# Optimization experiments

Hardware: AMD Instinct MI355X
Metric: run time of the kernel (lower is better)

The kernel has to match this reference:

```python
import jax, jax.numpy as jnp
import numpy as np

P, F_IN, HG, C, T, E, HOUT = 4096, 64, 64, 64, 32, 65536, 12
LEAKY_SLOPE = 0.2
LN_EPS = 1e-5


def setup_inputs() -> dict:
    key = jax.random.key(0)
    ks = jax.random.split(key, 14)
    g = lambda k, shape, scale: (jax.random.normal(k, shape, jnp.float32) * scale)
    return {
        "X": jax.random.normal(ks[0], (1, P, F_IN, T), jnp.float32),
        "edge_index": jax.random.randint(ks[1], (T, 2, E), 0, P, jnp.int32),
        # GATv2 params (single head)
        "Wl": g(ks[2], (F_IN, HG), 0.1),
        "Wr": g(ks[3], (F_IN, HG), 0.1),
        "att": g(ks[4], (HG,), 0.1),
        "gat_b": g(ks[5], (HG,), 0.02),
        # 1x1 time conv (HG -> C) and 1x1 residual conv (F_IN -> C)
        "W_time": g(ks[6], (C, HG), 0.1),
        "b_time": g(ks[7], (C,), 0.02),
        "W_res": g(ks[8], (C, F_IN), 0.1),
        "b_res": g(ks[9], (C,), 0.02),
        # LayerNorm over channel dim C
        "ln_g": jnp.ones((C,), jnp.float32),
        "ln_b": jnp.zeros((C,), jnp.float32),
        # final conv: Conv2d(in=T, out=HOUT, kernel=(1, C)) -> weight (HOUT, T, C)
        "W_final": g(ks[10], (HOUT, T, C), 0.05),
        "b_final": g(ks[11], (HOUT,), 0.02),
    }


def reference(X, edge_index, Wl, Wr, att, gat_b, W_time, b_time, W_res, b_res,
              ln_g, ln_b, W_final, b_final):
    Pn = X.shape[1]

    def gat_t(x, edges):
        # x: (P, F_IN), edges: (2, E) with edges[0]=src j, edges[1]=dst i
        src, dst = edges[0], edges[1]
        hl = x @ Wl                      # (P, HG) messages
        hr = x @ Wr                      # (P, HG) query side
        e = jax.nn.leaky_relu(hl[src] + hr[dst], LEAKY_SLOPE) @ att  # (E,)
        emax = jax.ops.segment_max(e, dst, num_segments=Pn)
        ex = jnp.exp(e - emax[dst])
        den = jax.ops.segment_sum(ex, dst, num_segments=Pn)
        alpha = ex / den[dst]            # softmax over in-edges of each dst
        return jax.ops.segment_sum(alpha[:, None] * hl[src], dst,
                                   num_segments=Pn) + gat_b  # (P, HG)

    xs = jnp.moveaxis(X[0], -1, 0)                     # (T, P, F_IN)
    X_hat = jax.nn.relu(jax.vmap(gat_t)(xs, edge_index))  # (T, P, HG)

    th = jnp.einsum('tph,ch->tpc', X_hat, W_time) + b_time  # time conv 1x1
    rs = jnp.einsum('tpf,cf->tpc', xs, W_res) + b_res       # residual conv 1x1
    y = jax.nn.relu(th + rs)                                 # (T, P, C)

    mu = jnp.mean(y, axis=-1, keepdims=True)
    var = jnp.var(y, axis=-1, keepdims=True)
    yn = (y - mu) * jax.lax.rsqrt(var + LN_EPS) * ln_g + ln_b  # (T, P, C)

    # final conv: in-channels = T, kernel (1, C) -> contract over t and c
    out = jnp.einsum('tpc,otc->po', yn, W_final) + b_final     # (P, HOUT)
    return out[None]                                           # (1, P, HOUT)
```

## Files before the change

### kernel.cpp

```cpp
#include <hip/hip_runtime.h>
#include <math.h>

#define NP 4096
#define F_IN 64
#define HG 64
#define NC 64
#define NT 32
#define NE 65536
#define HOUT 12
#define LEAKY 0.2f
#define LN_EPS 1e-5f
#define CAPC 32
#define XSP 2568

template <int CTRL>
__device__ __forceinline__ float dppadd(float v, float x) {
    int r = __builtin_amdgcn_update_dpp(0, __builtin_bit_cast(int, x), CTRL, 0xF, 0xF, false);
    return v + __builtin_bit_cast(float, r);
}
__device__ __forceinline__ float rowsum16(float v) {
    v = dppadd<0x128>(v, v);
    v = dppadd<0x124>(v, v);
    v = dppadd<0x122>(v, v);
    v = dppadd<0x121>(v, v);
    return v;
}
__device__ __forceinline__ float laneXorSum(float v) {
    v += __shfl_xor(v, 16, 64);
    v += __shfl_xor(v, 32, 64);
    return v;
}

#define FMA4(Acomp, B, r)                                                     \
    acc[r][0] += (Acomp) * (B).x; acc[r][1] += (Acomp) * (B).y;               \
    acc[r][2] += (Acomp) * (B).z; acc[r][3] += (Acomp) * (B).w;

__global__ __launch_bounds__(256) void k_front(const float* __restrict__ X,
        const float* __restrict__ Wl, const float* __restrict__ Wr,
        const float* __restrict__ W_res, const float* __restrict__ b_res,
        const float* __restrict__ bf,
        const int* __restrict__ EI,
        float* __restrict__ hl, float* __restrict__ hr, float* __restrict__ rs,
        float* __restrict__ out,
        int* __restrict__ cnt, unsigned short* __restrict__ scap) {
    __shared__ float smem[9488];
    int b = blockIdx.x;
    int tid = threadIdx.x;
    if (b < 512) {
        unsigned short (*buck)[CAPC] = (unsigned short (*)[CAPC])smem;
        int* cnts = (int*)(smem + 8192);
        int t = (b & 7) + 8 * ((b >> 3) & 3);
        int rem = b >> 5;
        int c = rem & 1, r = rem >> 1;
        cnts[tid] = 0; cnts[tid + 256] = 0;
        __syncthreads();
        const int4* srcA = (const int4*)(EI + (size_t)t * 2 * NE) + c * (NE / 8);
        const int4* dstA = (const int4*)(EI + (size_t)t * 2 * NE + NE) + c * (NE / 8);
        for (int i = tid; i < NE / 8; i += 256) {
            int4 s = srcA[i];
            int4 d = dstA[i];
            if ((d.x >> 9) == r) { int lo = d.x & 511; int sl = atomicAdd(&cnts[lo], 1); if (sl < CAPC) buck[lo][sl] = (unsigned short)s.x; }
            if ((d.y >> 9) == r) { int lo = d.y & 511; int sl = atomicAdd(&cnts[lo], 1); if (sl < CAPC) buck[lo][sl] = (unsigned short)s.y; }
            if ((d.z >> 9) == r) { int lo = d.z & 511; int sl = atomicAdd(&cnts[lo], 1); if (sl < CAPC) buck[lo][sl] = (unsigned short)s.z; }
            if ((d.w >> 9) == r) { int lo = d.w & 511; int sl = atomicAdd(&cnts[lo], 1); if (sl < CAPC) buck[lo][sl] = (unsigned short)s.w; }
        }
        __syncthreads();
        int obase = ((t * 2 + c) << 12) + (r << 9);
        cnt[obase + tid] = cnts[tid];
        cnt[obase + tid + 256] = cnts[tid + 256];
        unsigned int* dstw = (unsigned int*)(scap + (size_t)obase * CAPC);
        const unsigned int* srcw = (const unsigned int*)buck;
        for (int i = tid; i < 512 * CAPC / 2; i += 256)
            dstw[i] = srcw[i];
    } else if (b < 2560) {
        float* xs = smem;
        float (*bk)[68] = (float (*)[68])(smem + 2 * XSP);
        int p0 = (b - 512) * 2;
        const float4* Xp = (const float4*)(X + (size_t)p0 * F_IN * NT);
        for (int i4 = tid; i4 < 1024; i4 += 256) {
            int pp = i4 >> 9, f = (i4 >> 3) & 63, t0 = (i4 & 7) * 4;
            *(float4*)&xs[pp * XSP + f * 40 + t0] = Xp[i4];
        }
        int ng = tid & 15, pp = (tid >> 4) & 1, tg = tid >> 5;
        int n0 = ng * 4, t0 = tg * 4;
        int ppb = pp * XSP;
        {
            const float4* B4 = (const float4*)Wl;
            for (int i4 = tid; i4 < 1024; i4 += 256)
                *(float4*)&bk[i4 >> 4][(i4 & 15) * 4] = B4[i4];
            __syncthreads();
            float acc[4][4];
#pragma unroll
            for (int i = 0; i < 4; ++i)
#pragma unroll
                for (int j2 = 0; j2 < 4; ++j2) acc[i][j2] = 0.f;
#pragma unroll 8
            for (int f = 0; f < F_IN; ++f) {
                float4 B = *(const float4*)&bk[f][n0];
                float4 A = *(const float4*)&xs[ppb + f * 40 + t0];
                FMA4(A.x, B, 0) FMA4(A.y, B, 1) FMA4(A.z, B, 2) FMA4(A.w, B, 3)
            }
#pragma unroll
            for (int i = 0; i < 4; ++i) {
                float4 v;
                v.x = acc[i][0]; v.y = acc[i][1]; v.z = acc[i][2]; v.w = acc[i][3];
                *(float4*)&hl[((size_t)(t0 + i) * NP + p0 + pp) * HG + n0] = v;
            }
            __syncthreads();
        }
        {
            const float4* B4 = (const float4*)Wr;
            for (int i4 = tid; i4 < 1024; i4 += 256)
                *(float4*)&bk[i4 >> 4][(i4 & 15) * 4] = B4[i4];
            __syncthreads();
            float acc[4][4];
#pragma unroll
            for (int i = 0; i < 4; ++i)
#pragma unroll
                for (int j2 = 0; j2 < 4; ++j2) acc[i][j2] = 0.f;
#pragma unroll 8
            for (int f = 0; f < F_IN; ++f) {
                float4 B = *(const float4*)&bk[f][n0];
                float4 A = *(const float4*)&xs[ppb + f * 40 + t0];
                FMA4(A.x, B, 0) FMA4(A.y, B, 1) FMA4(A.z, B, 2) FMA4(A.w, B, 3)
            }
#pragma unroll
            for (int i = 0; i < 4; ++i) {
                float4 v;
                v.x = acc[i][0]; v.y = acc[i][1]; v.z = acc[i][2]; v.w = acc[i][3];
                *(float4*)&hr[((size_t)(t0 + i) * NP + p0 + pp) * HG + n0] = v;
            }
            __syncthreads();
        }
        {
            for (int i = tid; i < F_IN * NC; i += 256) {
                int c = i >> 6, f = i & 63;
                bk[f][c] = W_res[i];
            }
            __syncthreads();
            float4 br4 = *(const float4*)&b_res[n0];
            float acc[4][4];
#pragma unroll
            for (int i = 0; i < 4; ++i) {
                acc[i][0] = br4.x; acc[i][1] = br4.y; acc[i][2] = br4.z; acc[i][3] = br4.w;
            }
#pragma unroll 8
            for (int f = 0; f < F_IN; ++f) {
                float4 B = *(const float4*)&bk[f][n0];
                float4 A = *(const float4*)&xs[ppb + f * 40 + t0];
                FMA4(A.x, B, 0) FMA4(A.y, B, 1) FMA4(A.z, B, 2) FMA4(A.w, B, 3)
            }
#pragma unroll
            for (int i = 0; i < 4; ++i) {
                float4 v;
                v.x = acc[i][0]; v.y = acc[i][1]; v.z = acc[i][2]; v.w = acc[i][3];
                *(float4*)&rs[((size_t)(t0 + i) * NP + p0 + pp) * NC + n0] = v;
            }
        }
    } else {
        int i = (b - 2560) * 256 + tid;
        out[i] = bf[i % HOUT];
    }
}

__global__ __launch_bounds__(256, 8) void k_gat(const float* __restrict__ hl,
        float* __restrict__ hr,
        const int* __restrict__ cnt, const unsigned short* __restrict__ scap,
        const float* __restrict__ att, const float* __restrict__ gat_b) {
    __shared__ int sidx[4][72];
    int b = blockIdx.x;
    int k = b >> 3;
    int t = (b & 7) + 8 * (k >> 10);
    int ws = __builtin_amdgcn_readfirstlane(threadIdx.x >> 6);
    int i = (k & 1023) * 4 + ws;
    int lane = threadIdx.x & 63;
    int row = lane >> 4;
    int c0 = (lane & 15) * 4;
    const float* hlt = hl + (size_t)t * NP * HG;
    float4 at4 = *(const float4*)&att[c0];
    int d0 = cnt[((t * 2 + 0) << 12) + i]; d0 = (d0 < CAPC) ? d0 : CAPC;
    int d1 = cnt[((t * 2 + 1) << 12) + i]; d1 = (d1 < CAPC) ? d1 : CAPC;
    int deg = d0 + d1;
    const unsigned short* s0p = scap + ((size_t)(((t * 2 + 0) << 12) + i)) * CAPC;
    const unsigned short* s1p = scap + ((size_t)(((t * 2 + 1) << 12) + i)) * CAPC;
    int li = (lane < deg) ? lane : 0;
    int f1 = (li >= d0);
    int idx = f1 ? (li - d0) : li;
    sidx[ws][lane] = (int)(f1 ? s1p : s0p)[idx];
    if (lane < 8) sidx[ws][64 + lane] = 0;
    size_t nbase = ((size_t)t * NP + i) * HG;
    float4 r4 = *(const float4*)&hr[nbase + c0];
    int degp = (deg + 7) & ~7;
    float l = 0.f;
    float4 acc = {0.f, 0.f, 0.f, 0.f};
    float4 h0, h1;
    {
        int sa = sidx[ws][row];
        int sb = sidx[ws][4 + row];
        h0 = *(const float4*)&hlt[((size_t)sa << 6) + c0];
        h1 = *(const float4*)&hlt[((size_t)sb << 6) + c0];
    }
    for (int j = 0; j < degp; j += 8) {
        int na = sidx[ws][j + 8 + row];
        int nb = sidx[ws][j + 12 + row];
        float4 hn0 = *(const float4*)&hlt[((size_t)na << 6) + c0];
        float4 hn1 = *(const float4*)&hlt[((size_t)nb << 6) + c0];
        float4 z0, z1;
        z0.x = h0.x + r4.x; z0.y = h0.y + r4.y; z0.z = h0.z + r4.z; z0.w = h0.w + r4.w;
        z1.x = h1.x + r4.x; z1.y = h1.y + r4.y; z1.z = h1.z + r4.z; z1.w = h1.w + r4.w;
        z0.x = fmaxf(z0.x, LEAKY * z0.x); z0.y = fmaxf(z0.y, LEAKY * z0.y);
        z0.z = fmaxf(z0.z, LEAKY * z0.z); z0.w = fmaxf(z0.w, LEAKY * z0.w);
        z1.x = fmaxf(z1.x, LEAKY * z1.x); z1.y = fmaxf(z1.y, LEAKY * z1.y);
        z1.z = fmaxf(z1.z, LEAKY * z1.z); z1.w = fmaxf(z1.w, LEAKY * z1.w);
        float e0 = rowsum16(z0.x * at4.x + z0.y * at4.y + z0.z * at4.z + z0.w * at4.w);
        float e1 = rowsum16(z1.x * at4.x + z1.y * at4.y + z1.z * at4.z + z1.w * at4.w);
        float w0 = __expf(e0);
        float w1 = __expf(e1);
        w0 = (j + row < deg) ? w0 : 0.f;
        w1 = (j + 4 + row < deg) ? w1 : 0.f;
        l += w0 + w1;
        acc.x += w0 * h0.x + w1 * h1.x;
        acc.y += w0 * h0.y + w1 * h1.y;
        acc.z += w0 * h0.z + w1 * h1.z;
        acc.w += w0 * h0.w + w1 * h1.w;
        h0 = hn0; h1 = hn1;
    }
    float lt = laneXorSum(l);
    acc.x = laneXorSum(acc.x);
    acc.y = laneXorSum(acc.y);
    acc.z = laneXorSum(acc.z);
    acc.w = laneXorSum(acc.w);
    if (row == 0) {
        float inv = (deg > 0) ? (1.0f / lt) : 0.f;
        float4 gb = *(const float4*)&gat_b[c0];
        float4 o;
        o.x = fmaxf(acc.x * inv + gb.x, 0.f);
        o.y = fmaxf(acc.y * inv + gb.y, 0.f);
        o.z = fmaxf(acc.z * inv + gb.z, 0.f);
        o.w = fmaxf(acc.w * inv + gb.w, 0.f);
        *(float4*)&hr[nbase + c0] = o;
    }
}

__global__ __launch_bounds__(256) void k_pf(const float* __restrict__ Xhat,
        const float* __restrict__ W_time, const float* __restrict__ b_time,
        const float* __restrict__ rs, const float* __restrict__ ln_g,
        const float* __restrict__ ln_b, const float* __restrict__ Wf,
        float* __restrict__ out) {
    __shared__ float in_t[64][68];
    __shared__ float bk[64][68];
    int bx = blockIdx.x;
    int tc = bx & 7;
    int p0 = (bx >> 3) * 64;
    int tid = threadIdx.x;
    for (int i = tid; i < 4096; i += 256)
        bk[i & 63][i >> 6] = W_time[i];
    int cg = tid & 15, pg = tid >> 4;
    int c0 = cg * 4, pl = pg * 4;
    float4 bt4 = *(const float4*)&b_time[c0];
    float4 lg = *(const float4*)&ln_g[c0];
    float4 lb = *(const float4*)&ln_b[c0];
    float ot[4][HOUT];
#pragma unroll
    for (int i = 0; i < 4; ++i)
#pragma unroll
        for (int o = 0; o < HOUT; ++o) ot[i][o] = 0.f;
    float4 rg[4];
    {
        const float4* src = (const float4*)(Xhat + ((size_t)tc * NP + p0) * HG);
#pragma unroll
        for (int r = 0; r < 4; ++r) rg[r] = src[tid + 256 * r];
    }
    for (int ti = 0; ti < 4; ++ti) {
        int t = tc + ti * 8;
        __syncthreads();
#pragma unroll
        for (int r = 0; r < 4; ++r) {
            int i4 = tid + 256 * r;
            *(float4*)&in_t[i4 >> 4][(i4 & 15) * 4] = rg[r];
        }
        __syncthreads();
        if (ti < 3) {
            const float4* src = (const float4*)(Xhat + ((size_t)(t + 8) * NP + p0) * HG);
#pragma unroll
            for (int r = 0; r < 4; ++r) rg[r] = src[tid + 256 * r];
        }
        float acc[4][4];
#pragma unroll
        for (int i = 0; i < 4; ++i) {
            acc[i][0] = bt4.x; acc[i][1] = bt4.y; acc[i][2] = bt4.z; acc[i][3] = bt4.w;
        }
#pragma unroll
        for (int k4 = 0; k4 < 16; ++k4) {
            float4 A0 = *(const float4*)&in_t[pl + 0][k4 * 4];
            float4 A1 = *(const float4*)&in_t[pl + 1][k4 * 4];
            float4 A2 = *(const float4*)&in_t[pl + 2][k4 * 4];
            float4 A3 = *(const float4*)&in_t[pl + 3][k4 * 4];
            float4 B0 = *(const float4*)&bk[k4 * 4 + 0][c0];
            FMA4(A0.x, B0, 0) FMA4(A1.x, B0, 1) FMA4(A2.x, B0, 2) FMA4(A3.x, B0, 3)
            float4 B1 = *(const float4*)&bk[k4 * 4 + 1][c0];
            FMA4(A0.y, B1, 0) FMA4(A1.y, B1, 1) FMA4(A2.y, B1, 2) FMA4(A3.y, B1, 3)
            float4 B2 = *(const float4*)&bk[k4 * 4 + 2][c0];
            FMA4(A0.z, B2, 0) FMA4(A1.z, B2, 1) FMA4(A2.z, B2, 2) FMA4(A3.z, B2, 3)
            float4 B3 = *(const float4*)&bk[k4 * 4 + 3][c0];
            FMA4(A0.w, B3, 0) FMA4(A1.w, B3, 1) FMA4(A2.w, B3, 2) FMA4(A3.w, B3, 3)
        }
        float4 ynv[4];
#pragma unroll
        for (int i = 0; i < 4; ++i) {
            size_t prow = (size_t)t * NP + p0 + pl + i;
            float4 r4 = *(const float4*)&rs[prow * NC + c0];
            float y0 = fmaxf(acc[i][0] + r4.x, 0.f), y1 = fmaxf(acc[i][1] + r4.y, 0.f);
            float y2 = fmaxf(acc[i][2] + r4.z, 0.f), y3 = fmaxf(acc[i][3] + r4.w, 0.f);
            float s = rowsum16(y0 + y1 + y2 + y3);
            float ss = rowsum16(y0 * y0 + y1 * y1 + y2 * y2 + y3 * y3);
            float mu = s * (1.f / 64.f);
            float var = ss * (1.f / 64.f) - mu * mu;
            float rsd = rsqrtf(var + LN_EPS);
            ynv[i].x = (y0 - mu) * rsd * lg.x + lb.x;
            ynv[i].y = (y1 - mu) * rsd * lg.y + lb.y;
            ynv[i].z = (y2 - mu) * rsd * lg.z + lb.z;
            ynv[i].w = (y3 - mu) * rsd * lg.w + lb.w;
        }
#pragma unroll
        for (int o = 0; o < HOUT; ++o) {
            float4 w4 = *(const float4*)&Wf[(size_t)o * NT * NC + t * NC + c0];
#pragma unroll
            for (int i = 0; i < 4; ++i)
                ot[i][o] += ynv[i].x * w4.x + ynv[i].y * w4.y
                          + ynv[i].z * w4.z + ynv[i].w * w4.w;
        }
    }
#pragma unroll
    for (int i = 0; i < 4; ++i)
#pragma unroll
        for (int o = 0; o < HOUT; ++o) ot[i][o] = rowsum16(ot[i][o]);
    if (cg == 0) {
#pragma unroll
        for (int i = 0; i < 4; ++i) {
            int p = p0 + pl + i;
#pragma unroll
            for (int o = 0; o < HOUT; ++o)
                atomicAdd(&out[p * HOUT + o], ot[i][o]);
        }
    }
}

extern "C" void kernel_launch(void* const* d_in, const int* in_sizes, int n_in,
                              void* d_out, int out_size, void* d_ws, size_t ws_size,
                              hipStream_t stream) {
    const float* X      = (const float*)d_in[0];
    const int*   EI     = (const int*)d_in[1];
    const float* Wl     = (const float*)d_in[2];
    const float* Wr     = (const float*)d_in[3];
    const float* att    = (const float*)d_in[4];
    const float* gat_b  = (const float*)d_in[5];
    const float* W_time = (const float*)d_in[6];
    const float* b_time = (const float*)d_in[7];
    const float* W_res  = (const float*)d_in[8];
    const float* b_res  = (const float*)d_in[9];
    const float* ln_g   = (const float*)d_in[10];
    const float* ln_b   = (const float*)d_in[11];
    const float* Wf     = (const float*)d_in[12];
    const float* bf     = (const float*)d_in[13];
    float* out = (float*)d_out;

    char* ws = (char*)d_ws;
    const size_t MB = 1024 * 1024;
    float* hl   = (float*)(ws);
    float* hr   = (float*)(ws + 32 * MB);
    float* rs   = (float*)(ws + 64 * MB);
    int*   cnt  = (int*)  (ws + 96 * MB);
    unsigned short* scap = (unsigned short*)(ws + 97 * MB);

    k_front<<<2752, 256, 0, stream>>>(X, Wl, Wr, W_res, b_res, bf, EI,
                                      hl, hr, rs, out, cnt, scap);
    k_gat  <<<(NT * NP) / 4, 256, 0, stream>>>(hl, hr, cnt, scap, att, gat_b);
    k_pf   <<<512, 256, 0, stream>>>(hr, W_time, b_time, rs, ln_g, ln_b, Wf, out);
}
```

Before: 273.0 us.

## Fuse GAT aggregation into post-GAT time-conv/LayerNorm/final-conv kernel

Merges the GAT attention kernel and the post-processing kernel into one. Each block computes GAT outputs for 64 nodes at a given timestep straight into shared memory, then applies the time conv, residual, LayerNorm and final projection. This drops the global round trip of X_hat and one kernel launch. The cost is fewer blocks (1024 instead of 32768 GAT blocks) and serial per-wave node loops, so there is less parallelism for hiding gather latency.

Result: slower. 331.2 us (+21.3%).

```diff
diff --git a/kernel.cpp b/kernel.cpp
--- a/kernel.cpp
+++ b/kernel.cpp
@@ -163,128 +163,107 @@
     }
 }
 
-__global__ __launch_bounds__(256, 8) void k_gat(const float* __restrict__ hl,
-        float* __restrict__ hr,
+__global__ __launch_bounds__(256) void k_gpf(const float* __restrict__ hl,
+        const float* __restrict__ hr, const float* __restrict__ rs,
         const int* __restrict__ cnt, const unsigned short* __restrict__ scap,
-        const float* __restrict__ att, const float* __restrict__ gat_b) {
-    __shared__ int sidx[4][72];
-    int b = blockIdx.x;
-    int k = b >> 3;
-    int t = (b & 7) + 8 * (k >> 10);
-    int ws = __builtin_amdgcn_readfirstlane(threadIdx.x >> 6);
-    int i = (k & 1023) * 4 + ws;
-    int lane = threadIdx.x & 63;
-    int row = lane >> 4;
-    int c0 = (lane & 15) * 4;
-    const float* hlt = hl + (size_t)t * NP * HG;
-    float4 at4 = *(const float4*)&att[c0];
-    int d0 = cnt[((t * 2 + 0) << 12) + i]; d0 = (d0 < CAPC) ? d0 : CAPC;
-    int d1 = cnt[((t * 2 + 1) << 12) + i]; d1 = (d1 < CAPC) ? d1 : CAPC;
-    int deg = d0 + d1;
-    const unsigned short* s0p = scap + ((size_t)(((t * 2 + 0) << 12) + i)) * CAPC;
-    const unsigned short* s1p = scap + ((size_t)(((t * 2 + 1) << 12) + i)) * CAPC;
-    int li = (lane < deg) ? lane : 0;
-    int f1 = (li >= d0);
-    int idx = f1 ? (li - d0) : li;
-    sidx[ws][lane] = (int)(f1 ? s1p : s0p)[idx];
-    if (lane < 8) sidx[ws][64 + lane] = 0;
-    size_t nbase = ((size_t)t * NP + i) * HG;
-    float4 r4 = *(const float4*)&hr[nbase + c0];
-    int degp = (deg + 7) & ~7;
-    float l = 0.f;
-    float4 acc = {0.f, 0.f, 0.f, 0.f};
-    float4 h0, h1;
-    {
-        int sa = sidx[ws][row];
-        int sb = sidx[ws][4 + row];
-        h0 = *(const float4*)&hlt[((size_t)sa << 6) + c0];
-        h1 = *(const float4*)&hlt[((size_t)sb << 6) + c0];
-    }
-    for (int j = 0; j < degp; j += 8) {
-        int na = sidx[ws][j + 8 + row];
-        int nb = sidx[ws][j + 12 + row];
-        float4 hn0 = *(const float4*)&hlt[((size_t)na << 6) + c0];
-        float4 hn1 = *(const float4*)&hlt[((size_t)nb << 6) + c0];
-        float4 z0, z1;
-        z0.x = h0.x + r4.x; z0.y = h0.y + r4.y; z0.z = h0.z + r4.z; z0.w = h0.w + r4.w;
-        z1.x = h1.x + r4.x; z1.y = h1.y + r4.y; z1.z = h1.z + r4.z; z1.w = h1.w + r4.w;
-        z0.x = fmaxf(z0.x, LEAKY * z0.x); z0.y = fmaxf(z0.y, LEAKY * z0.y);
-        z0.z = fmaxf(z0.z, LEAKY * z0.z); z0.w = fmaxf(z0.w, LEAKY * z0.w);
-        z1.x = fmaxf(z1.x, LEAKY * z1.x); z1.y = fmaxf(z1.y, LEAKY * z1.y);
-        z1.z = fmaxf(z1.z, LEAKY * z1.z); z1.w = fmaxf(z1.w, LEAKY * z1.w);
-        float e0 = rowsum16(z0.x * at4.x + z0.y * at4.y + z0.z * at4.z + z0.w * at4.w);
-        float e1 = rowsum16(z1.x * at4.x + z1.y * at4.y + z1.z * at4.z + z1.w * at4.w);
-        float w0 = __expf(e0);
-        float w1 = __expf(e1);
-        w0 = (j + row < deg) ? w0 : 0.f;
-        w1 = (j + 4 + row < deg) ? w1 : 0.f;
-        l += w0 + w1;
-        acc.x += w0 * h0.x + w1 * h1.x;
-        acc.y += w0 * h0.y + w1 * h1.y;
-        acc.z += w0 * h0.z + w1 * h1.z;
-        acc.w += w0 * h0.w + w1 * h1.w;
-        h0 = hn0; h1 = hn1;
-    }
-    float lt = laneXorSum(l);
-    acc.x = laneXorSum(acc.x);
-    acc.y = laneXorSum(acc.y);
-    acc.z = laneXorSum(acc.z);
-    acc.w = laneXorSum(acc.w);
-    if (row == 0) {
-        float inv = (deg > 0) ? (1.0f / lt) : 0.f;
-        float4 gb = *(const float4*)&gat_b[c0];
-        float4 o;
-        o.x = fmaxf(acc.x * inv + gb.x, 0.f);
-        o.y = fmaxf(acc.y * inv + gb.y, 0.f);
-        o.z = fmaxf(acc.z * inv + gb.z, 0.f);
-        o.w = fmaxf(acc.w * inv + gb.w, 0.f);
-        *(float4*)&hr[nbase + c0] = o;
-    }
-}
-
-__global__ __launch_bounds__(256) void k_pf(const float* __restrict__ Xhat,
+        const float* __restrict__ att, const float* __restrict__ gat_b,
         const float* __restrict__ W_time, const float* __restrict__ b_time,
-        const float* __restrict__ rs, const float* __restrict__ ln_g,
-        const float* __restrict__ ln_b, const float* __restrict__ Wf,
-        float* __restrict__ out) {
+        const float* __restrict__ ln_g, const float* __restrict__ ln_b,
+        const float* __restrict__ Wf, float* __restrict__ out) {
     __shared__ float in_t[64][68];
     __shared__ float bk[64][68];
+    __shared__ int sidx[4][72];
     int bx = blockIdx.x;
-    int tc = bx & 7;
-    int p0 = (bx >> 3) * 64;
+    int tc = bx & 15;
+    int p0 = (bx >> 4) * 64;
     int tid = threadIdx.x;
+    int ws = __builtin_amdgcn_readfirstlane(tid >> 6);
+    int lane = tid & 63;
+    int row = lane >> 4;
+    int cg = lane & 15;
+    int c0 = cg * 4;
     for (int i = tid; i < 4096; i += 256)
         bk[i & 63][i >> 6] = W_time[i];
-    int cg = tid & 15, pg = tid >> 4;
-    int c0 = cg * 4, pl = pg * 4;
+    float4 at4 = *(const float4*)&att[c0];
+    float4 gb4 = *(const float4*)&gat_b[c0];
     float4 bt4 = *(const float4*)&b_time[c0];
-    float4 lg = *(const float4*)&ln_g[c0];
-    float4 lb = *(const float4*)&ln_b[c0];
+    float4 lg  = *(const float4*)&ln_g[c0];
+    float4 lb  = *(const float4*)&ln_b[c0];
+    int pg = tid >> 4, pl = pg * 4;
     float ot[4][HOUT];
 #pragma unroll
     for (int i = 0; i < 4; ++i)
 #pragma unroll
         for (int o = 0; o < HOUT; ++o) ot[i][o] = 0.f;
-    float4 rg[4];
-    {
-        const float4* src = (const float4*)(Xhat + ((size_t)tc * NP + p0) * HG);
-#pragma unroll
-        for (int r = 0; r < 4; ++r) rg[r] = src[tid + 256 * r];
-    }
-    for (int ti = 0; ti < 4; ++ti) {
-        int t = tc + ti * 8;
+
+    for (int ti = 0; ti < 2; ++ti) {
+        int t = tc + 16 * ti;
+        const float* hlt = hl + (size_t)t * NP * HG;
+        for (int q = 0; q < 16; ++q) {
+            int plocal = ws * 16 + q;
+            int p = p0 + plocal;
+            int d0 = cnt[((t * 2 + 0) << 12) + p]; d0 = (d0 < CAPC) ? d0 : CAPC;
+            int d1 = cnt[((t * 2 + 1) << 12) + p]; d1 = (d1 < CAPC) ? d1 : CAPC;
+            int deg = d0 + d1;
+            const unsigned short* s0p = scap + ((size_t)(((t * 2 + 0) << 12) + p)) * CAPC;
+            const unsigned short* s1p = scap + ((size_t)(((t * 2 + 1) << 12) + p)) * CAPC;
+            int li = (lane < deg) ? lane : 0;
+            int f1 = (li >= d0);
+            int idx = f1 ? (li - d0) : li;
+            sidx[ws][lane] = (int)(f1 ? s1p : s0p)[idx];
+            if (lane < 8) sidx[ws][64 + lane] = 0;
+            float4 r4 = *(const float4*)&hr[((size_t)t * NP + p) * HG + c0];
+            int degp = (deg + 7) & ~7;
+            float l = 0.f;
+            float4 acc = {0.f, 0.f, 0.f, 0.f};
+            float4 h0, h1;
+            {
+                int sa = sidx[ws][row];
+                int sb = sidx[ws][4 + row];
+                h0 = *(const float4*)&hlt[((size_t)sa << 6) + c0];
+                h1 = *(const float4*)&hlt[((size_t)sb << 6) + c0];
+            }
+            for (int j = 0; j < degp; j += 8) {
+                int na = sidx[ws][j + 8 + row];
+                int nb = sidx[ws][j + 12 + row];
+                float4 hn0 = *(const float4*)&hlt[((size_t)na << 6) + c0];
+                float4 hn1 = *(const float4*)&hlt[((size_t)nb << 6) + c0];
+                float4 z0, z1;
+                z0.x = h0.x + r4.x; z0.y = h0.y + r4.y; z0.z = h0.z + r4.z; z0.w = h0.w + r4.w;
+                z1.x = h1.x + r4.x; z1.y = h1.y + r4.y; z1.z = h1.z + r4.z; z1.w = h1.w + r4.w;
+                z0.x = fmaxf(z0.x, LEAKY * z0.x); z0.y = fmaxf(z0.y, LEAKY * z0.y);
+                z0.z = fmaxf(z0.z, LEAKY * z0.z); z0.w = fmaxf(z0.w, LEAKY * z0.w);
+                z1.x = fmaxf(z1.x, LEAKY * z1.x); z1.y = fmaxf(z1.y, LEAKY * z1.y);
+                z1.z = fmaxf(z1.z, LEAKY * z1.z); z1.w = fmaxf(z1.w, LEAKY * z1.w);
+                float e0 = rowsum16(z0.x * at4.x + z0.y * at4.y + z0.z * at4.z + z0.w * at4.w);
+                float e1 = rowsum16(z1.x * at4.x + z1.y * at4.y + z1.z * at4.z + z1.w * at4.w);
+                float w0 = __expf(e0);
+                float w1 = __expf(e1);
+                w0 = (j + row < deg) ? w0 : 0.f;
+                w1 = (j + 4 + row < deg) ? w1 : 0.f;
+                l += w0 + w1;
+                acc.x += w0 * h0.x + w1 * h1.x;
+                acc.y += w0 * h0.y + w1 * h1.y;
+                acc.z += w0 * h0.z + w1 * h1.z;
+                acc.w += w0 * h0.w + w1 * h1.w;
+                h0 = hn0; h1 = hn1;
+            }
+            float lt = laneXorSum(l);
+            acc.x = laneXorSum(acc.x);
+            acc.y = laneXorSum(acc.y);
+            acc.z = laneXorSum(acc.z);
+            acc.w = laneXorSum(acc.w);
+            if (row == 0) {
+                float inv = (deg > 0) ? (1.0f / lt) : 0.f;
+                float4 o4;
+                o4.x = fmaxf(acc.x * inv + gb4.x, 0.f);
+                o4.y = fmaxf(acc.y * inv + gb4.y, 0.f);
+                o4.z = fmaxf(acc.z * inv + gb4.z, 0.f);
+                o4.w = fmaxf(acc.w * inv + gb4.w, 0.f);
+                *(float4*)&in_t[plocal][c0] = o4;
+            }
+        }
         __syncthreads();
-#pragma unroll
-        for (int r = 0; r < 4; ++r) {
-            int i4 = tid + 256 * r;
-            *(float4*)&in_t[i4 >> 4][(i4 & 15) * 4] = rg[r];
-        }
-        __syncthreads();
-        if (ti < 3) {
-            const float4* src = (const float4*)(Xhat + ((size_t)(t + 8) * NP + p0) * HG);
-#pragma unroll
-            for (int r = 0; r < 4; ++r) rg[r] = src[tid + 256 * r];
-        }
         float acc[4][4];
 #pragma unroll
         for (int i = 0; i < 4; ++i) {
@@ -330,6 +309,7 @@
                 ot[i][o] += ynv[i].x * w4.x + ynv[i].y * w4.y
                           + ynv[i].z * w4.z + ynv[i].w * w4.w;
         }
+        __syncthreads();
     }
 #pragma unroll
     for (int i = 0; i < 4; ++i)
@@ -375,6 +355,6 @@
 
     k_front<<<2752, 256, 0, stream>>>(X, Wl, Wr, W_res, b_res, bf, EI,
                                       hl, hr, rs, out, cnt, scap);
-    k_gat  <<<(NT * NP) / 4, 256, 0, stream>>>(hl, hr, cnt, scap, att, gat_b);
-    k_pf   <<<512, 256, 0, stream>>>(hr, W_time, b_time, rs, ln_g, ln_b, Wf, out);
-}
+    k_gpf  <<<1024, 256, 0, stream>>>(hl, hr, rs, cnt, scap, att, gat_b,
+                                      W_time, b_time, ln_g, ln_b, Wf, out);
+}
```
